# Optimization experiments

Hardware: AMD Instinct MI355X
Metric: run time of the kernel (lower is better)

Reference implementation:

```python
import jax, jax.numpy as jnp
import numpy as np

N, D, E = 10000, 64, 32768   # nodes, padded degree, target edges
F, H, O = 64, 256, 1         # in_channels, hidden_channels, out_channels


def _linear_init(key, fin, fout):
    kw, kb = jax.random.split(key)
    s = 1.0 / np.sqrt(fin)
    w = jax.random.uniform(kw, (fin, fout), jnp.float32, -s, s)
    b = jax.random.uniform(kb, (fout,), jnp.float32, -s, s)
    return w, b


def setup_inputs() -> dict:
    key = jax.random.key(0)
    ks = jax.random.split(key, 12)
    x = jax.random.normal(ks[0], (N, F), jnp.float32)
    adj_nbr = jax.random.randint(ks[1], (N, D), 0, N)          # padded neighbor lists
    tar_ei = jax.random.randint(ks[2], (2, E), 0, N)           # target edges
    xcn_w1, xcn_b1 = _linear_init(ks[3], F, H)
    xcn_w2, xcn_b2 = _linear_init(ks[4], H, H)
    xcn_w3, xcn_b3 = _linear_init(ks[5], H, H)
    xij_w1, xij_b1 = _linear_init(ks[6], F, H)
    xij_w2, xij_b2 = _linear_init(ks[7], H, H)
    lin_w1, lin_b1 = _linear_init(ks[8], H, H)
    lin_w2, lin_b2 = _linear_init(ks[9], H, O)
    beta = jnp.ones((1,), jnp.float32)
    return dict(x=x, adj_nbr=adj_nbr, tar_ei=tar_ei, beta=beta,
                xcn_w1=xcn_w1, xcn_b1=xcn_b1, xcn_w2=xcn_w2, xcn_b2=xcn_b2,
                xcn_w3=xcn_w3, xcn_b3=xcn_b3,
                xij_w1=xij_w1, xij_b1=xij_b1, xij_w2=xij_w2, xij_b2=xij_b2,
                lin_w1=lin_w1, lin_b1=lin_b1, lin_w2=lin_w2, lin_b2=lin_b2)


def reference(x, adj_nbr, tar_ei, beta,
              xcn_w1, xcn_b1, xcn_w2, xcn_b2, xcn_w3, xcn_b3,
              xij_w1, xij_b1, xij_w2, xij_b2,
              lin_w1, lin_b1, lin_w2, lin_b2):
    relu = jax.nn.relu
    i, j = tar_ei[0], tar_ei[1]
    # adjoverlap: common-neighbor intersection of rows i and j of the adjacency
    ni = adj_nbr[i]                                   # [E, D] neighbors of i
    nj = adj_nbr[j]                                   # [E, D] neighbors of j
    cm = (ni[:, :, None] == nj[:, None, :]).any(-1)   # [E, D] ni[a] in N(j)?
    # spmm_add(cn, x): sum features of common neighbors per target edge
    xcn = jnp.einsum('ed,edf->ef', cm.astype(x.dtype), x[ni])  # [E, F]
    # xijlin(xi * xj): Linear -> ReLU -> Linear
    xij = x[i] * x[j]
    h_ij = relu(xij @ xij_w1 + xij_b1) @ xij_w2 + xij_b2
    # xcnlin(xcn): Linear -> ReLU -> Linear -> ReLU -> Linear
    h_cn = relu(xcn @ xcn_w1 + xcn_b1)
    h_cn = relu(h_cn @ xcn_w2 + xcn_b2)
    h_cn = h_cn @ xcn_w3 + xcn_b3
    # lin(xcnlin(xcn) * beta + xij): Linear -> ReLU -> Linear
    h = relu((h_cn * beta + h_ij) @ lin_w1 + lin_b1)
    return h @ lin_w2 + lin_b2                        # [E, O]
```

## Files before the change

### kernel.cpp

```cpp
#include <hip/hip_runtime.h>

#define NNODES 10000
#define DDEG   64
#define NEDGES 32768
#define FIN    64
#define HID    256

typedef __attribute__((ext_vector_type(8))) __bf16 bf16x8;
typedef __attribute__((ext_vector_type(4))) float  f32x4;

__device__ __forceinline__ unsigned short f2bf(float f) {
    unsigned x = __float_as_uint(f);
    return (unsigned short)((x + 0x7FFFu + ((x >> 16) & 1u)) >> 16);
}
__device__ __forceinline__ float b2f(unsigned short u) {
    return __uint_as_float(((unsigned)u) << 16);
}

#define OFF_XIJ1 0
#define OFF_XIJ2 16384
#define OFF_XCN1 81920
#define OFF_XCN2 98304
#define OFF_XCN3 163840
#define OFF_LIN1 229376
#define WT_TOTAL 294912
#define NTILES   36

__host__ __device__ constexpr int tile_off(int t) {
    return t < 2  ? OFF_XIJ1 + t * 8192
         : t < 10 ? OFF_XIJ2 + (t - 2) * 8192
         : t < 12 ? OFF_XCN1 + (t - 10) * 8192
         : t < 20 ? OFF_XCN2 + (t - 12) * 8192
         : t < 28 ? OFF_XCN3 + (t - 20) * 8192
         :          OFF_LIN1 + (t - 28) * 8192;
}

__global__ __launch_bounds__(256) void prep_k(const float* __restrict__ xij_w1,
                                              const float* __restrict__ xij_w2,
                                              const float* __restrict__ xcn_w1,
                                              const float* __restrict__ xcn_w2,
                                              const float* __restrict__ xcn_w3,
                                              const float* __restrict__ lin_w1,
                                              unsigned short* __restrict__ WT) {
    int idx = blockIdx.x * 256 + threadIdx.x;
    const float* src;
    int r;
    if (idx < OFF_XIJ2)      { r = idx - OFF_XIJ1; src = xij_w1; }
    else if (idx < OFF_XCN1) { r = idx - OFF_XIJ2; src = xij_w2; }
    else if (idx < OFF_XCN2) { r = idx - OFF_XCN1; src = xcn_w1; }
    else if (idx < OFF_XCN3) { r = idx - OFF_XCN2; src = xcn_w2; }
    else if (idx < OFF_LIN1) { r = idx - OFF_XCN3; src = xcn_w3; }
    else                     { r = idx - OFF_LIN1; src = lin_w1; }
    int kb  = r >> 13;
    int n   = (r & 8191) >> 5;
    int klo = r & 31;
    WT[idx] = f2bf(src[(kb * 32 + klo) * HID + n]);
}

__device__ __forceinline__ void gll16(const unsigned short* g, unsigned short* l) {
    __builtin_amdgcn_global_load_lds(
        (const __attribute__((address_space(1))) unsigned int*)g,
        (__attribute__((address_space(3))) unsigned int*)l, 16, 0, 0);
}
__device__ __forceinline__ void stage_tile(const unsigned short* g, unsigned short* l,
                                           int tid, int wv) {
#pragma unroll
    for (int c = 0; c < 2; ++c)
        gll16(g + c * 4096 + tid * 8, l + c * 4096 + wv * 512);
}

template <int T0, int NT, int LDA>
__device__ __forceinline__ void run_phase(const unsigned short* As,
                                          unsigned short* ring,
                                          const unsigned short* __restrict__ WT,
                                          int lr, int lg, int col0, int r0,
                                          int tid, int wv, f32x4 acc[4][4]) {
#pragma unroll
    for (int m = 0; m < 4; ++m)
#pragma unroll
        for (int n = 0; n < 4; ++n) acc[m][n] = (f32x4){0.f, 0.f, 0.f, 0.f};
    const int sw = (lr & 7) << 3;
#pragma unroll
    for (int s = 0; s < NT; ++s) {
        const int t = T0 + s;
        if (t < NTILES - 1)
            asm volatile("s_waitcnt vmcnt(2) lgkmcnt(0)" ::: "memory");
        else
            asm volatile("s_waitcnt vmcnt(0) lgkmcnt(0)" ::: "memory");
        __builtin_amdgcn_s_barrier();
        const unsigned short* cur = ring + (t % 3) * 8192;
        bf16x8 a[4], b[4];
#pragma unroll
        for (int n = 0; n < 4; ++n)
            b[n] = *reinterpret_cast<const bf16x8*>(&cur[(col0 + n * 16 + lr) * 32 + 8 * lg]);
#pragma unroll
        for (int m = 0; m < 4; ++m)
            a[m] = *reinterpret_cast<const bf16x8*>(
                &As[(r0 + m * 16 + lr) * LDA + ((s * 32 + 8 * lg) ^ sw)]);
        __builtin_amdgcn_s_setprio(1);
#pragma unroll
        for (int m = 0; m < 4; ++m)
#pragma unroll
            for (int n = 0; n < 4; ++n)
                acc[m][n] = __builtin_amdgcn_mfma_f32_16x16x32_bf16(a[m], b[n], acc[m][n], 0, 0, 0);
        __builtin_amdgcn_s_setprio(0);
        if (t + 2 < NTILES)
            stage_tile(WT + tile_off(t + 2), ring + ((t + 2) % 3) * 8192, tid, wv);
    }
}

__global__ __launch_bounds__(512, 1) void fused_k(const float* __restrict__ x,
                                                  const int* __restrict__ adj,
                                                  const int* __restrict__ tar,
                                                  const unsigned short* __restrict__ WT,
                                                  const float* __restrict__ xij_b1,
                                                  const float* __restrict__ xij_b2,
                                                  const float* __restrict__ xcn_b1,
                                                  const float* __restrict__ xcn_b2,
                                                  const float* __restrict__ xcn_b3,
                                                  const float* __restrict__ lin_b1,
                                                  const float* __restrict__ lin_w2,
                                                  const float* __restrict__ lin_b2,
                                                  const float* __restrict__ beta,
                                                  float* __restrict__ out) {
    __shared__ unsigned short sXij[128 * 64];
    __shared__ unsigned short sXcn[128 * 64];
    __shared__ unsigned short sH[128 * 256];
    __shared__ unsigned short sB[3 * 8192];

    const int tid  = threadIdx.x;
    const int wv   = tid >> 6;
    const int lane = tid & 63;
    const int lr   = lane & 15;
    const int lg   = lane >> 4;
    const int r0   = (wv >> 2) * 64;
    const int col0 = (wv & 3) * 64;
    const int row0 = blockIdx.x * 128;

    stage_tile(WT + tile_off(0), sB, tid, wv);
    stage_tile(WT + tile_off(1), sB + 8192, tid, wv);
    const float betaf = beta[0];

    {
        const int e0 = row0 + wv * 16;
        int   ic = tar[e0];
        int   jc = tar[NEDGES + e0];
        int   ni_c = adj[ic * DDEG + lane];
        int   nj_c = adj[jc * DDEG + lane];
        float xi_c = x[ic * FIN + lane];
        float xj_c = x[jc * FIN + lane];
        for (int t = 0; t < 16; ++t) {
            int ni = ni_c, nj = nj_c;
            float xi = xi_c, xj = xj_c;
            if (t < 15) {
                int e = e0 + t + 1;
                int i2 = tar[e];
                int j2 = tar[NEDGES + e];
                ni_c = adj[i2 * DDEG + lane];
                nj_c = adj[j2 * DDEG + lane];
                xi_c = x[i2 * FIN + lane];
                xj_c = x[j2 * FIN + lane];
            }
            bool found = false;
#pragma unroll
            for (int b = 0; b < 64; ++b)
                found |= (ni == (int)__builtin_amdgcn_readlane(nj, b));
            unsigned long long m = __ballot(found);
            float acc = 0.f;
            while (m) {
                int a = __ffsll(m) - 1;
                m &= m - 1;
                int r = (int)__builtin_amdgcn_readlane(ni, a);
                acc += x[r * FIN + lane];
            }
            int el = wv * 16 + t;
            int sidx = el * FIN + (lane ^ ((el & 7) << 3));
            sXij[sidx] = f2bf(xi * xj);
            sXcn[sidx] = f2bf(acc);
        }
    }

    f32x4 acc[4][4];
    float bl[4];

    run_phase<0, 2, 64>(sXij, sB, WT, lr, lg, col0, r0, tid, wv, acc);
#pragma unroll
    for (int n = 0; n < 4; ++n) bl[n] = xij_b1[col0 + n * 16 + lr];
#pragma unroll
    for (int m = 0; m < 4; ++m)
#pragma unroll
        for (int n = 0; n < 4; ++n)
#pragma unroll
            for (int i = 0; i < 4; ++i) {
                int row = r0 + m * 16 + 4 * lg + i;
                int col = col0 + n * 16 + lr;
                sH[row * HID + (col ^ ((row & 7) << 3))] = f2bf(fmaxf(acc[m][n][i] + bl[n], 0.f));
            }

    run_phase<2, 8, 256>(sH, sB, WT, lr, lg, col0, r0, tid, wv, acc);
#pragma unroll
    for (int n = 0; n < 4; ++n) bl[n] = xij_b2[col0 + n * 16 + lr];
    unsigned hij_lo[4][4], hij_hi[4][4];
#pragma unroll
    for (int m = 0; m < 4; ++m)
#pragma unroll
        for (int n = 0; n < 4; ++n) {
            hij_lo[m][n] = ((unsigned)f2bf(acc[m][n][1] + bl[n]) << 16) | f2bf(acc[m][n][0] + bl[n]);
            hij_hi[m][n] = ((unsigned)f2bf(acc[m][n][3] + bl[n]) << 16) | f2bf(acc[m][n][2] + bl[n]);
        }

    run_phase<10, 2, 64>(sXcn, sB, WT, lr, lg, col0, r0, tid, wv, acc);
#pragma unroll
    for (int n = 0; n < 4; ++n) bl[n] = xcn_b1[col0 + n * 16 + lr];
#pragma unroll
    for (int m = 0; m < 4; ++m)
#pragma unroll
        for (int n = 0; n < 4; ++n)
#pragma unroll
            for (int i = 0; i < 4; ++i) {
                int row = r0 + m * 16 + 4 * lg + i;
                int col = col0 + n * 16 + lr;
                sH[row * HID + (col ^ ((row & 7) << 3))] = f2bf(fmaxf(acc[m][n][i] + bl[n], 0.f));
            }

    run_phase<12, 8, 256>(sH, sB, WT, lr, lg, col0, r0, tid, wv, acc);
    asm volatile("s_waitcnt lgkmcnt(0)" ::: "memory");
    __builtin_amdgcn_s_barrier();
#pragma unroll
    for (int n = 0; n < 4; ++n) bl[n] = xcn_b2[col0 + n * 16 + lr];
#pragma unroll
    for (int m = 0; m < 4; ++m)
#pragma unroll
        for (int n = 0; n < 4; ++n)
#pragma unroll
            for (int i = 0; i < 4; ++i) {
                int row = r0 + m * 16 + 4 * lg + i;
                int col = col0 + n * 16 + lr;
                sH[row * HID + (col ^ ((row & 7) << 3))] = f2bf(fmaxf(acc[m][n][i] + bl[n], 0.f));
            }

    run_phase<20, 8, 256>(sH, sB, WT, lr, lg, col0, r0, tid, wv, acc);
    asm volatile("s_waitcnt lgkmcnt(0)" ::: "memory");
    __builtin_amdgcn_s_barrier();
#pragma unroll
    for (int n = 0; n < 4; ++n) bl[n] = xcn_b3[col0 + n * 16 + lr];
#pragma unroll
    for (int m = 0; m < 4; ++m)
#pragma unroll
        for (int n = 0; n < 4; ++n) {
            float h0 = b2f((unsigned short)(hij_lo[m][n] & 0xFFFF));
            float h1 = b2f((unsigned short)(hij_lo[m][n] >> 16));
            float h2 = b2f((unsigned short)(hij_hi[m][n] & 0xFFFF));
            float h3 = b2f((unsigned short)(hij_hi[m][n] >> 16));
            float v0 = (acc[m][n][0] + bl[n]) * betaf + h0;
            float v1 = (acc[m][n][1] + bl[n]) * betaf + h1;
            float v2 = (acc[m][n][2] + bl[n]) * betaf + h2;
            float v3 = (acc[m][n][3] + bl[n]) * betaf + h3;
            int rb = r0 + m * 16 + 4 * lg;
            int col = col0 + n * 16 + lr;
            sH[(rb + 0) * HID + (col ^ (((rb + 0) & 7) << 3))] = f2bf(v0);
            sH[(rb + 1) * HID + (col ^ (((rb + 1) & 7) << 3))] = f2bf(v1);
            sH[(rb + 2) * HID + (col ^ (((rb + 2) & 7) << 3))] = f2bf(v2);
            sH[(rb + 3) * HID + (col ^ (((rb + 3) & 7) << 3))] = f2bf(v3);
        }

    run_phase<28, 8, 256>(sH, sB, WT, lr, lg, col0, r0, tid, wv, acc);
#pragma unroll
    for (int n = 0; n < 4; ++n) bl[n] = lin_b1[col0 + n * 16 + lr];
    float w2l[4];
#pragma unroll
    for (int n = 0; n < 4; ++n) w2l[n] = lin_w2[col0 + n * 16 + lr];
    float* sRed = (float*)sXij;
#pragma unroll
    for (int m = 0; m < 4; ++m) {
        float p[4] = {0.f, 0.f, 0.f, 0.f};
#pragma unroll
        for (int n = 0; n < 4; ++n)
#pragma unroll
            for (int i = 0; i < 4; ++i)
                p[i] += fmaxf(acc[m][n][i] + bl[n], 0.f) * w2l[n];
#pragma unroll
        for (int i = 0; i < 4; ++i) {
            float s = p[i];
            s += __shfl_xor(s, 1);
            s += __shfl_xor(s, 2);
            s += __shfl_xor(s, 4);
            s += __shfl_xor(s, 8);
            if (lr == 0) sRed[(wv & 3) * 128 + r0 + m * 16 + 4 * lg + i] = s;
        }
    }
    __syncthreads();
    if (tid < 128)
        out[row0 + tid] = sRed[tid] + sRed[128 + tid] + sRed[256 + tid] + sRed[384 + tid] + lin_b2[0];
}

extern "C" void kernel_launch(void* const* d_in, const int* in_sizes, int n_in,
                              void* d_out, int out_size, void* d_ws, size_t ws_size,
                              hipStream_t stream) {
    const float* x      = (const float*)d_in[0];
    const int*   adj    = (const int*)d_in[1];
    const int*   tar    = (const int*)d_in[2];
    const float* beta   = (const float*)d_in[3];
    const float* xcn_w1 = (const float*)d_in[4];
    const float* xcn_b1 = (const float*)d_in[5];
    const float* xcn_w2 = (const float*)d_in[6];
    const float* xcn_b2 = (const float*)d_in[7];
    const float* xcn_w3 = (const float*)d_in[8];
    const float* xcn_b3 = (const float*)d_in[9];
    const float* xij_w1 = (const float*)d_in[10];
    const float* xij_b1 = (const float*)d_in[11];
    const float* xij_w2 = (const float*)d_in[12];
    const float* xij_b2 = (const float*)d_in[13];
    const float* lin_w1 = (const float*)d_in[14];
    const float* lin_b1 = (const float*)d_in[15];
    const float* lin_w2 = (const float*)d_in[16];
    const float* lin_b2 = (const float*)d_in[17];

    unsigned short* WT = (unsigned short*)d_ws;

    prep_k<<<WT_TOTAL / 256, 256, 0, stream>>>(xij_w1, xij_w2, xcn_w1, xcn_w2, xcn_w3, lin_w1, WT);
    fused_k<<<NEDGES / 128, 512, 0, stream>>>(x, adj, tar, WT,
                                              xij_b1, xij_b2, xcn_b1, xcn_b2, xcn_b3,
                                              lin_b1, lin_w2, lin_b2, beta, (float*)d_out);
}
```

Before: 72.43 us.

## Split edge gather/intersection into a separate high-occupancy kernel with weight prep

Moves the common-neighbour intersection and feature gather out of the single-block-per-CU MLP kernel into a new kernel with one wave per edge and many small blocks, merging the weight bf16 conversion into it. The MLP kernel now streams pre-swizzled bf16 edge features from global memory into LDS. It also issues the next weight tile prefetch right after the barrier instead of after the MFMAs. This trades an extra global round-trip of the edge features (about 8 MB) for much higher latency hiding on the irregular gather phase.

```diff
diff --git a/kernel.cpp b/kernel.cpp
--- a/kernel.cpp
+++ b/kernel.cpp
@@ -35,28 +35,6 @@
          :          OFF_LIN1 + (t - 28) * 8192;
 }
 
-__global__ __launch_bounds__(256) void prep_k(const float* __restrict__ xij_w1,
-                                              const float* __restrict__ xij_w2,
-                                              const float* __restrict__ xcn_w1,
-                                              const float* __restrict__ xcn_w2,
-                                              const float* __restrict__ xcn_w3,
-                                              const float* __restrict__ lin_w1,
-                                              unsigned short* __restrict__ WT) {
-    int idx = blockIdx.x * 256 + threadIdx.x;
-    const float* src;
-    int r;
-    if (idx < OFF_XIJ2)      { r = idx - OFF_XIJ1; src = xij_w1; }
-    else if (idx < OFF_XCN1) { r = idx - OFF_XIJ2; src = xij_w2; }
-    else if (idx < OFF_XCN2) { r = idx - OFF_XCN1; src = xcn_w1; }
-    else if (idx < OFF_XCN3) { r = idx - OFF_XCN2; src = xcn_w2; }
-    else if (idx < OFF_LIN1) { r = idx - OFF_XCN3; src = xcn_w3; }
-    else                     { r = idx - OFF_LIN1; src = lin_w1; }
-    int kb  = r >> 13;
-    int n   = (r & 8191) >> 5;
-    int klo = r & 31;
-    WT[idx] = f2bf(src[(kb * 32 + klo) * HID + n]);
-}
-
 __device__ __forceinline__ void gll16(const unsigned short* g, unsigned short* l) {
     __builtin_amdgcn_global_load_lds(
         (const __attribute__((address_space(1))) unsigned int*)g,
@@ -67,6 +45,63 @@
 #pragma unroll
     for (int c = 0; c < 2; ++c)
         gll16(g + c * 4096 + tid * 8, l + c * 4096 + wv * 512);
+}
+
+__global__ __launch_bounds__(256) void edge_prep_k(const float* __restrict__ x,
+                                                   const int* __restrict__ adj,
+                                                   const int* __restrict__ tar,
+                                                   const float* __restrict__ xij_w1,
+                                                   const float* __restrict__ xij_w2,
+                                                   const float* __restrict__ xcn_w1,
+                                                   const float* __restrict__ xcn_w2,
+                                                   const float* __restrict__ xcn_w3,
+                                                   const float* __restrict__ lin_w1,
+                                                   unsigned short* __restrict__ WT,
+                                                   unsigned short* __restrict__ xij_g,
+                                                   unsigned short* __restrict__ xcn_g) {
+    const int wv   = threadIdx.x >> 6;
+    const int lane = threadIdx.x & 63;
+    const int e    = blockIdx.x * 4 + wv;
+
+    int i = tar[e];
+    int j = tar[NEDGES + e];
+    int ni = adj[i * DDEG + lane];
+    int nj = adj[j * DDEG + lane];
+    float xi = x[i * FIN + lane];
+    float xj = x[j * FIN + lane];
+
+    bool found = false;
+#pragma unroll
+    for (int b = 0; b < 64; ++b)
+        found |= (ni == (int)__builtin_amdgcn_readlane(nj, b));
+    unsigned long long m = __ballot(found);
+
+    float acc = 0.f;
+    while (m) {
+        int a = __ffsll(m) - 1;
+        m &= m - 1;
+        int r = (int)__builtin_amdgcn_readlane(ni, a);
+        acc += x[r * FIN + lane];
+    }
+    int sl = lane ^ ((e & 7) << 3);
+    xij_g[(size_t)e * FIN + sl] = f2bf(xi * xj);
+    xcn_g[(size_t)e * FIN + sl] = f2bf(acc);
+
+    if (blockIdx.x < WT_TOTAL / 256) {
+        int idx = blockIdx.x * 256 + threadIdx.x;
+        const float* src;
+        int r;
+        if (idx < OFF_XIJ2)      { r = idx - OFF_XIJ1; src = xij_w1; }
+        else if (idx < OFF_XCN1) { r = idx - OFF_XIJ2; src = xij_w2; }
+        else if (idx < OFF_XCN2) { r = idx - OFF_XCN1; src = xcn_w1; }
+        else if (idx < OFF_XCN3) { r = idx - OFF_XCN2; src = xcn_w2; }
+        else if (idx < OFF_LIN1) { r = idx - OFF_XCN3; src = xcn_w3; }
+        else                     { r = idx - OFF_LIN1; src = lin_w1; }
+        int kb  = r >> 13;
+        int n   = (r & 8191) >> 5;
+        int klo = r & 31;
+        WT[idx] = f2bf(src[(kb * 32 + klo) * HID + n]);
+    }
 }
 
 template <int T0, int NT, int LDA>
@@ -88,6 +123,8 @@
         else
             asm volatile("s_waitcnt vmcnt(0) lgkmcnt(0)" ::: "memory");
         __builtin_amdgcn_s_barrier();
+        if (t + 2 < NTILES)
+            stage_tile(WT + tile_off(t + 2), ring + ((t + 2) % 3) * 8192, tid, wv);
         const unsigned short* cur = ring + (t % 3) * 8192;
         bf16x8 a[4], b[4];
 #pragma unroll
@@ -104,25 +141,22 @@
             for (int n = 0; n < 4; ++n)
                 acc[m][n] = __builtin_amdgcn_mfma_f32_16x16x32_bf16(a[m], b[n], acc[m][n], 0, 0, 0);
         __builtin_amdgcn_s_setprio(0);
-        if (t + 2 < NTILES)
-            stage_tile(WT + tile_off(t + 2), ring + ((t + 2) % 3) * 8192, tid, wv);
     }
 }
 
-__global__ __launch_bounds__(512, 1) void fused_k(const float* __restrict__ x,
-                                                  const int* __restrict__ adj,
-                                                  const int* __restrict__ tar,
-                                                  const unsigned short* __restrict__ WT,
-                                                  const float* __restrict__ xij_b1,
-                                                  const float* __restrict__ xij_b2,
-                                                  const float* __restrict__ xcn_b1,
-                                                  const float* __restrict__ xcn_b2,
-                                                  const float* __restrict__ xcn_b3,
-                                                  const float* __restrict__ lin_b1,
-                                                  const float* __restrict__ lin_w2,
-                                                  const float* __restrict__ lin_b2,
-                                                  const float* __restrict__ beta,
-                                                  float* __restrict__ out) {
+__global__ __launch_bounds__(512, 1) void mlp_k(const unsigned short* __restrict__ xij_g,
+                                                const unsigned short* __restrict__ xcn_g,
+                                                const unsigned short* __restrict__ WT,
+                                                const float* __restrict__ xij_b1,
+                                                const float* __restrict__ xij_b2,
+                                                const float* __restrict__ xcn_b1,
+                                                const float* __restrict__ xcn_b2,
+                                                const float* __restrict__ xcn_b3,
+                                                const float* __restrict__ lin_b1,
+                                                const float* __restrict__ lin_w2,
+                                                const float* __restrict__ lin_b2,
+                                                const float* __restrict__ beta,
+                                                float* __restrict__ out) {
     __shared__ unsigned short sXij[128 * 64];
     __shared__ unsigned short sXcn[128 * 64];
     __shared__ unsigned short sH[128 * 256];
@@ -137,48 +171,11 @@
     const int col0 = (wv & 3) * 64;
     const int row0 = blockIdx.x * 128;
 
+    stage_tile(xij_g + (size_t)row0 * FIN, sXij, tid, wv);
+    stage_tile(xcn_g + (size_t)row0 * FIN, sXcn, tid, wv);
     stage_tile(WT + tile_off(0), sB, tid, wv);
     stage_tile(WT + tile_off(1), sB + 8192, tid, wv);
     const float betaf = beta[0];
-
-    {
-        const int e0 = row0 + wv * 16;
-        int   ic = tar[e0];
-        int   jc = tar[NEDGES + e0];
-        int   ni_c = adj[ic * DDEG + lane];
-        int   nj_c = adj[jc * DDEG + lane];
-        float xi_c = x[ic * FIN + lane];
-        float xj_c = x[jc * FIN + lane];
-        for (int t = 0; t < 16; ++t) {
-            int ni = ni_c, nj = nj_c;
-            float xi = xi_c, xj = xj_c;
-            if (t < 15) {
-                int e = e0 + t + 1;
-                int i2 = tar[e];
-                int j2 = tar[NEDGES + e];
-                ni_c = adj[i2 * DDEG + lane];
-                nj_c = adj[j2 * DDEG + lane];
-                xi_c = x[i2 * FIN + lane];
-                xj_c = x[j2 * FIN + lane];
-            }
-            bool found = false;
-#pragma unroll
-            for (int b = 0; b < 64; ++b)
-                found |= (ni == (int)__builtin_amdgcn_readlane(nj, b));
-            unsigned long long m = __ballot(found);
-            float acc = 0.f;
-            while (m) {
-                int a = __ffsll(m) - 1;
-                m &= m - 1;
-                int r = (int)__builtin_amdgcn_readlane(ni, a);
-                acc += x[r * FIN + lane];
-            }
-            int el = wv * 16 + t;
-            int sidx = el * FIN + (lane ^ ((el & 7) << 3));
-            sXij[sidx] = f2bf(xi * xj);
-            sXcn[sidx] = f2bf(acc);
-        }
-    }
 
     f32x4 acc[4][4];
     float bl[4];
@@ -316,10 +313,14 @@
     const float* lin_w2 = (const float*)d_in[16];
     const float* lin_b2 = (const float*)d_in[17];
 
-    unsigned short* WT = (unsigned short*)d_ws;
-
-    prep_k<<<WT_TOTAL / 256, 256, 0, stream>>>(xij_w1, xij_w2, xcn_w1, xcn_w2, xcn_w3, lin_w1, WT);
-    fused_k<<<NEDGES / 128, 512, 0, stream>>>(x, adj, tar, WT,
-                                              xij_b1, xij_b2, xcn_b1, xcn_b2, xcn_b3,
-                                              lin_b1, lin_w2, lin_b2, beta, (float*)d_out);
-}
+    unsigned short* WT    = (unsigned short*)d_ws;
+    unsigned short* xij_g = (unsigned short*)((char*)d_ws + 589824);
+    unsigned short* xcn_g = (unsigned short*)((char*)d_ws + 4784128);
+
+    edge_prep_k<<<NEDGES / 4, 256, 0, stream>>>(x, adj, tar,
+                                                xij_w1, xij_w2, xcn_w1, xcn_w2, xcn_w3, lin_w1,
+                                                WT, xij_g, xcn_g);
+    mlp_k<<<NEDGES / 128, 512, 0, stream>>>(xij_g, xcn_g, WT,
+                                            xij_b1, xij_b2, xcn_b1, xcn_b2, xcn_b3,
+                                            lin_b1, lin_w2, lin_b2, beta, (float*)d_out);
+}
```

New measurement: 62.60 us. 13.6% less time.
